# Kernel tuning notes

Hardware: AMD Instinct MI355X
Metric: run time of the kernel (lower is better)

## Reference

```python
import jax, jax.numpy as jnp
import numpy as np

T = 4.0          # kd_T
PATCH_NUM = 16
MASK_NUM = 4
P = PATCH_NUM - MASK_NUM  # 12
B = 4096
D_IN = 640
D = 128


def embed(x, w1, b1, w2, b2):
    # Linear -> ReLU -> Linear -> L2 normalize over features
    h = jax.nn.relu(x @ w1.T + b1)
    y = h @ w2.T + b2
    norm = jnp.sqrt(jnp.sum(y * y, axis=1, keepdims=True))
    return y / norm


def kl_rows(y_s, y_t):
    # Matches KLDiv: kl_div(log_softmax(y_s/T), softmax(y_t/T), 'batchmean') * T^2
    # over dim=0 of a 1-D vector -> sum / D. Vectorized over leading dims.
    ls = jax.nn.log_softmax(y_s / T, axis=-1)
    lt = jax.nn.log_softmax(y_t / T, axis=-1)
    pt = jnp.exp(lt)
    return jnp.sum(pt * (lt - ls), axis=-1) / y_s.shape[-1] * (T * T)


def setup_inputs() -> dict:
    key = jax.random.key(0)
    ks = jax.random.split(key, 11)
    return {
        "ebg": jax.random.normal(ks[0], (B, D_IN), jnp.float32),
        "ebp": jax.random.normal(ks[1], (P * B, D_IN), jnp.float32),
        "labelsg": jax.random.randint(ks[2], (B,), 0, 64),
        "glo_w1": jax.random.normal(ks[3], (D, D_IN), jnp.float32) * 0.04,
        "glo_b1": jax.random.normal(ks[4], (D,), jnp.float32) * 0.02,
        "glo_w2": jax.random.normal(ks[5], (D, D), jnp.float32) * 0.09,
        "glo_b2": jax.random.normal(ks[6], (D,), jnp.float32) * 0.02,
        "pat_w1": jax.random.normal(ks[7], (D, D_IN), jnp.float32) * 0.04,
        "pat_b1": jax.random.normal(ks[8], (D,), jnp.float32) * 0.02,
        "pat_w2": jax.random.normal(ks[9], (D, D), jnp.float32) * 0.09,
        "pat_b2": jax.random.normal(ks[10], (D,), jnp.float32) * 0.02,
    }


def reference(ebg, ebp, labelsg, glo_w1, glo_b1, glo_w2, glo_b2,
              pat_w1, pat_b1, pat_w2, pat_b2):
    sg = jax.lax.stop_gradient
    g = embed(ebg, glo_w1, glo_b1, glo_w2, glo_b2)          # [B, D]
    p = embed(ebp, pat_w1, pat_b1, pat_w2, pat_b2)          # [P*B, D]
    p = p.reshape(P, B, D)
    p_bar = p.mean(axis=0)                                  # [B, D]

    # soft_dil_loss: symmetric KL between g[b] and p_bar[b]
    dil = jnp.sum(kl_rows(g, sg(p_bar)) + kl_rows(p_bar, sg(g)))

    # soft_dcl_loss: symmetric KL between (g[b]-p[b,l])^2 and (p_bar[b]-p[b,l])^2
    p_bt = jnp.transpose(p, (1, 0, 2))                      # [B, P, D]
    d1 = (g[:, None, :] - p_bt) ** 2                        # [B, P, D]
    d2 = (p_bar[:, None, :] - p_bt) ** 2                    # [B, P, D]
    dcl = jnp.sum(kl_rows(d1, sg(d2)) + kl_rows(d2, sg(d1))) / P

    return (dil, dcl)
```

## Files before the change

### kernel.cpp

```cpp
#include <hip/hip_runtime.h>
#include <math.h>

#define B_    4096
#define DIN   640
#define DD    128
#define PP    12
#define INV_T 0.25f

typedef __bf16 bft;
typedef __attribute__((ext_vector_type(8))) __bf16 bf16x8;
typedef __attribute__((ext_vector_type(4))) float fx4;

__global__ __launch_bounds__(256) void prep_kernel(
    const float* __restrict__ gw1, const float* __restrict__ pw1,
    const float* __restrict__ gw2, const float* __restrict__ pw2,
    bft* __restrict__ w1hg, bft* __restrict__ w1lg,
    bft* __restrict__ w1hp, bft* __restrict__ w1lp,
    bft* __restrict__ w2hg, bft* __restrict__ w2lg,
    bft* __restrict__ w2hp, bft* __restrict__ w2lp)
{
  int idx = blockIdx.x * 256 + threadIdx.x;
  const float* src; bft *dh, *dl; int off;
  if (idx < 81920)       { src = gw1; dh = w1hg; dl = w1lg; off = idx; }
  else if (idx < 163840) { src = pw1; dh = w1hp; dl = w1lp; off = idx - 81920; }
  else if (idx < 180224) { src = gw2; dh = w2hg; dl = w2lg; off = idx - 163840; }
  else                   { src = pw2; dh = w2hp; dl = w2lp; off = idx - 180224; }
  float x = src[off];
  bft h = (bft)x;
  dh[off] = h;
  dl[off] = (bft)(x - (float)h);
}

__global__ __launch_bounds__(256, 2) void embed_kernel(
    const float* __restrict__ ebg, const float* __restrict__ ebp,
    const bft* __restrict__ w1hg, const bft* __restrict__ w1lg, const float* __restrict__ b1g,
    const bft* __restrict__ w2hg, const bft* __restrict__ w2lg, const float* __restrict__ b2g,
    const bft* __restrict__ w1hp, const bft* __restrict__ w1lp, const float* __restrict__ b1p,
    const bft* __restrict__ w2hp, const bft* __restrict__ w2lp, const float* __restrict__ b2p,
    float* __restrict__ outg, float* __restrict__ outp)
{
  __shared__ bft hsm[2 * 128 * 128];
  bft* hhi = hsm;
  bft* hlo = hsm + 128 * 128;
  float* halfsq = (float*)hsm;

  const int t = threadIdx.x;
  const int w = t >> 6, lane = t & 63;
  const int wm = w >> 1, wn = w & 1;
  const int ln = lane & 15, quad = lane >> 4;

  const float *X, *B1, *B2;
  const bft *W1H, *W1L, *W2H, *W2L;
  float* Y;
  long m0;
  if (blockIdx.x < 32) {
    X = ebg; W1H = w1hg; W1L = w1lg; B1 = b1g; W2H = w2hg; W2L = w2lg; B2 = b2g;
    Y = outg; m0 = (long)blockIdx.x * 128;
  } else {
    X = ebp; W1H = w1hp; W1L = w1lp; B1 = b1p; W2H = w2hp; W2L = w2lp; B2 = b2p;
    Y = outp; m0 = (long)(blockIdx.x - 32) * 128;
  }

  const float* px[4];
#pragma unroll
  for (int mt = 0; mt < 4; mt++)
    px[mt] = X + (size_t)(m0 + wm * 64 + mt * 16 + ln) * DIN + quad * 8;

  const bft *p1h[4], *p1l[4];
#pragma unroll
  for (int nt = 0; nt < 4; nt++) {
    int n = wn * 64 + nt * 16 + ln;
    p1h[nt] = W1H + (size_t)n * DIN + quad * 8;
    p1l[nt] = W1L + (size_t)n * DIN + quad * 8;
  }

  fx4 acc[4][4];
#pragma unroll
  for (int mt = 0; mt < 4; mt++)
#pragma unroll
    for (int nt = 0; nt < 4; nt++) acc[mt][nt] = (fx4){0.f, 0.f, 0.f, 0.f};

#define LOADX(xlo, xhi, koff)                              \
  _Pragma("unroll")                                        \
  for (int mt = 0; mt < 4; mt++) {                         \
    xlo[mt] = *(const fx4*)(px[mt] + (koff));              \
    xhi[mt] = *(const fx4*)(px[mt] + (koff) + 4);          \
  }

#define LOADW(wh, wl, koff)                                \
  _Pragma("unroll")                                        \
  for (int nt = 0; nt < 4; nt++) {                         \
    wh[nt] = *(const bf16x8*)(p1h[nt] + (koff));           \
    wl[nt] = *(const bf16x8*)(p1l[nt] + (koff));           \
  }

#define PH1CHUNK(xlo, xhi, wh, wl)                                                     \
  {                                                                                    \
    bf16x8 ah[4], al[4];                                                               \
    _Pragma("unroll")                                                                  \
    for (int mt = 0; mt < 4; mt++) {                                                   \
      _Pragma("unroll")                                                                \
      for (int j = 0; j < 4; j++) {                                                    \
        float xv = xlo[mt][j];                                                         \
        bft hh = (bft)xv;                                                              \
        ah[mt][j] = hh;                                                                \
        al[mt][j] = (bft)(xv - (float)hh);                                             \
        float yv = xhi[mt][j];                                                         \
        bft hh2 = (bft)yv;                                                             \
        ah[mt][4 + j] = hh2;                                                           \
        al[mt][4 + j] = (bft)(yv - (float)hh2);                                        \
      }                                                                                \
    }                                                                                  \
    _Pragma("unroll")                                                                  \
    for (int mt = 0; mt < 4; mt++)                                                     \
      _Pragma("unroll")                                                                \
      for (int nt = 0; nt < 4; nt++) {                                                 \
        acc[mt][nt] = __builtin_amdgcn_mfma_f32_16x16x32_bf16(ah[mt], wh[nt], acc[mt][nt], 0, 0, 0); \
        acc[mt][nt] = __builtin_amdgcn_mfma_f32_16x16x32_bf16(al[mt], wh[nt], acc[mt][nt], 0, 0, 0); \
        acc[mt][nt] = __builtin_amdgcn_mfma_f32_16x16x32_bf16(ah[mt], wl[nt], acc[mt][nt], 0, 0, 0); \
      }                                                                                \
  }

  fx4 xla[4], xha[4], xlb[4], xhb[4];
  bf16x8 wha[4], wla[4], whb[4], wlb[4];
  LOADX(xla, xha, 0)
  LOADW(wha, wla, 0)
#pragma unroll 1
  for (int kc = 0; kc < 20; kc += 2) {
    const int k1 = (kc + 1) * 32;
    LOADX(xlb, xhb, k1)
    LOADW(whb, wlb, k1)
    PH1CHUNK(xla, xha, wha, wla)
    if (kc < 18) {
      const int k2 = (kc + 2) * 32;
      LOADX(xla, xha, k2)
      LOADW(wha, wla, k2)
    }
    PH1CHUNK(xlb, xhb, whb, wlb)
  }

#pragma unroll
  for (int nt = 0; nt < 4; nt++) {
    float bv = B1[wn * 64 + nt * 16 + ln];
    int c8 = wn * 8 + nt * 2 + (ln >> 3);
    int c7 = ln & 7;
#pragma unroll
    for (int mt = 0; mt < 4; mt++) {
#pragma unroll
      for (int r = 0; r < 4; r++) {
        float v = fmaxf(acc[mt][nt][r] + bv, 0.f);
        bft h = (bft)v;
        bft l = (bft)(v - (float)h);
        int m = wm * 64 + mt * 16 + quad * 4 + r;
        int addr = m * 128 + ((c8 ^ (m & 15)) << 3) + c7;
        hhi[addr] = h;
        hlo[addr] = l;
      }
    }
  }

  const bft *p2h[4], *p2l[4];
#pragma unroll
  for (int nt = 0; nt < 4; nt++) {
    int n = wn * 64 + nt * 16 + ln;
    p2h[nt] = W2H + (size_t)n * DD + quad * 8;
    p2l[nt] = W2L + (size_t)n * DD + quad * 8;
  }
  fx4 acc2[4][4];
#pragma unroll
  for (int nt = 0; nt < 4; nt++) {
    float bv = B2[wn * 64 + nt * 16 + ln];
#pragma unroll
    for (int mt = 0; mt < 4; mt++) acc2[mt][nt] = (fx4){bv, bv, bv, bv};
  }

#define LOADW2(wh, wl, koff)                               \
  _Pragma("unroll")                                        \
  for (int nt = 0; nt < 4; nt++) {                         \
    wh[nt] = *(const bf16x8*)(p2h[nt] + (koff));           \
    wl[nt] = *(const bf16x8*)(p2l[nt] + (koff));           \
  }

#define PH2CHUNK(kcv, wh, wl)                                                          \
  {                                                                                    \
    bf16x8 ah2[4], al2[4];                                                             \
    _Pragma("unroll")                                                                  \
    for (int mt = 0; mt < 4; mt++) {                                                   \
      int m = wm * 64 + mt * 16 + ln;                                                  \
      int c8 = ((kcv) * 4 + quad) ^ (m & 15);                                          \
      ah2[mt] = *(const bf16x8*)&hhi[m * 128 + (c8 << 3)];                             \
      al2[mt] = *(const bf16x8*)&hlo[m * 128 + (c8 << 3)];                             \
    }                                                                                  \
    _Pragma("unroll")                                                                  \
    for (int mt = 0; mt < 4; mt++)                                                     \
      _Pragma("unroll")                                                                \
      for (int nt = 0; nt < 4; nt++) {                                                 \
        acc2[mt][nt] = __builtin_amdgcn_mfma_f32_16x16x32_bf16(ah2[mt], wh[nt], acc2[mt][nt], 0, 0, 0); \
        acc2[mt][nt] = __builtin_amdgcn_mfma_f32_16x16x32_bf16(al2[mt], wh[nt], acc2[mt][nt], 0, 0, 0); \
        acc2[mt][nt] = __builtin_amdgcn_mfma_f32_16x16x32_bf16(ah2[mt], wl[nt], acc2[mt][nt], 0, 0, 0); \
      }                                                                                \
  }

  bf16x8 q2ha[4], q2la[4], q2hb[4], q2lb[4];
  LOADW2(q2ha, q2la, 0)
  __syncthreads();
  LOADW2(q2hb, q2lb, 32)
  PH2CHUNK(0, q2ha, q2la)
  LOADW2(q2ha, q2la, 64)
  PH2CHUNK(1, q2hb, q2lb)
  LOADW2(q2hb, q2lb, 96)
  PH2CHUNK(2, q2ha, q2la)
  PH2CHUNK(3, q2hb, q2lb)
  __syncthreads();

#pragma unroll
  for (int mt = 0; mt < 4; mt++) {
#pragma unroll
    for (int r = 0; r < 4; r++) {
      float s = 0.f;
#pragma unroll
      for (int nt = 0; nt < 4; nt++) { float v = acc2[mt][nt][r]; s += v * v; }
      s += __shfl_xor(s, 1, 64);
      s += __shfl_xor(s, 2, 64);
      s += __shfl_xor(s, 4, 64);
      s += __shfl_xor(s, 8, 64);
      if (ln == 0) halfsq[(wm * 64 + mt * 16 + quad * 4 + r) * 2 + wn] = s;
    }
  }
  __syncthreads();
#pragma unroll
  for (int mt = 0; mt < 4; mt++) {
#pragma unroll
    for (int r = 0; r < 4; r++) {
      int row = wm * 64 + mt * 16 + quad * 4 + r;
      float rinv = 1.0f / sqrtf(halfsq[row * 2] + halfsq[row * 2 + 1]);
#pragma unroll
      for (int nt = 0; nt < 4; nt++)
        Y[(m0 + row) * DD + wn * 64 + nt * 16 + ln] = acc2[mt][nt][r] * rinv;
    }
  }
}

__device__ __forceinline__ float sym_kl_row(float au0, float au1, float av0, float av1)
{
  float eu0 = __expf(au0), eu1 = __expf(au1);
  float ev0 = __expf(av0), ev1 = __expf(av1);
  float su = eu0 + eu1, sv = ev0 + ev1;
#pragma unroll
  for (int o = 32; o > 0; o >>= 1) {
    su += __shfl_xor(su, o, 64);
    sv += __shfl_xor(sv, o, 64);
  }
  float ru = 1.0f / su, rv = 1.0f / sv;
  float d0 = au0 - av0, d1 = au1 - av1;
  float part = (eu0 * ru - ev0 * rv) * d0 + (eu1 * ru - ev1 * rv) * d1;
#pragma unroll
  for (int o = 32; o > 0; o >>= 1) part += __shfl_xor(part, o, 64);
  return part;
}

__global__ __launch_bounds__(256) void loss_kernel(
    const float* __restrict__ g, const float* __restrict__ p,
    float* __restrict__ pdil, float* __restrict__ pdcl)
{
  __shared__ float wd[4], wc[4];
  int w = threadIdx.x >> 6, lane = threadIdx.x & 63;
  int b = blockIdx.x * 4 + w;
  float2 pl[PP];
  float sx = 0.f, sy = 0.f;
#pragma unroll
  for (int l = 0; l < PP; l++) {
    pl[l] = *(const float2*)&p[((size_t)l * B_ + b) * DD + lane * 2];
    sx += pl[l].x; sy += pl[l].y;
  }
  sx *= (1.0f / PP); sy *= (1.0f / PP);
  float2 gv = *(const float2*)&g[(size_t)b * DD + lane * 2];

  float dil = sym_kl_row(gv.x * INV_T, gv.y * INV_T, sx * INV_T, sy * INV_T) * 0.125f;

  float dcl = 0.f;
#pragma unroll
  for (int l = 0; l < PP; l++) {
    float u0 = (gv.x - pl[l].x) * (gv.x - pl[l].x) * INV_T;
    float u1 = (gv.y - pl[l].y) * (gv.y - pl[l].y) * INV_T;
    float v0 = (sx - pl[l].x) * (sx - pl[l].x) * INV_T;
    float v1 = (sy - pl[l].y) * (sy - pl[l].y) * INV_T;
    dcl += sym_kl_row(u0, u1, v0, v1);
  }
  dcl *= (1.0f / 96.0f);

  if (lane == 0) { wd[w] = dil; wc[w] = dcl; }
  __syncthreads();
  if (threadIdx.x == 0) pdil[blockIdx.x] = wd[0] + wd[1] + wd[2] + wd[3];
  if (threadIdx.x == 1) pdcl[blockIdx.x] = wc[0] + wc[1] + wc[2] + wc[3];
}

__global__ __launch_bounds__(256) void final_kernel(const float* __restrict__ pdil,
                                                    const float* __restrict__ pdcl,
                                                    float* __restrict__ out)
{
  __shared__ float red[8];
  int t = threadIdx.x;
  float s0 = 0.f, s1 = 0.f;
  for (int i = t; i < 1024; i += 256) { s0 += pdil[i]; s1 += pdcl[i]; }
#pragma unroll
  for (int o = 32; o > 0; o >>= 1) {
    s0 += __shfl_xor(s0, o, 64);
    s1 += __shfl_xor(s1, o, 64);
  }
  int wid = t >> 6, lane = t & 63;
  if (lane == 0) { red[wid] = s0; red[4 + wid] = s1; }
  __syncthreads();
  if (t == 0) out[0] = red[0] + red[1] + red[2] + red[3];
  if (t == 1) out[1] = red[4] + red[5] + red[6] + red[7];
}

extern "C" void kernel_launch(void* const* d_in, const int* in_sizes, int n_in,
                              void* d_out, int out_size, void* d_ws, size_t ws_size,
                              hipStream_t stream)
{
  const float* ebg = (const float*)d_in[0];
  const float* ebp = (const float*)d_in[1];
  const float* gw1 = (const float*)d_in[3];
  const float* gb1 = (const float*)d_in[4];
  const float* gw2 = (const float*)d_in[5];
  const float* gb2 = (const float*)d_in[6];
  const float* pw1 = (const float*)d_in[7];
  const float* pb1 = (const float*)d_in[8];
  const float* pw2 = (const float*)d_in[9];
  const float* pb2 = (const float*)d_in[10];
  float* out = (float*)d_out;

  float* ws   = (float*)d_ws;
  float* g    = ws;
  float* p    = g + (size_t)B_ * DD;
  float* pdil = p + (size_t)PP * B_ * DD;
  float* pdcl = pdil + 1024;
  bft* wb     = (bft*)(pdcl + 1024);
  bft* w1hg = wb;                 bft* w1lg = w1hg + 81920;
  bft* w1hp = w1lg + 81920;       bft* w1lp = w1hp + 81920;
  bft* w2hg = w1lp + 81920;       bft* w2lg = w2hg + 16384;
  bft* w2hp = w2lg + 16384;       bft* w2lp = w2hp + 16384;

  prep_kernel<<<768, 256, 0, stream>>>(gw1, pw1, gw2, pw2,
                                       w1hg, w1lg, w1hp, w1lp,
                                       w2hg, w2lg, w2hp, w2lp);
  embed_kernel<<<416, 256, 0, stream>>>(ebg, ebp,
                                        w1hg, w1lg, gb1, w2hg, w2lg, gb2,
                                        w1hp, w1lp, pb1, w2hp, w2lp, pb2,
                                        g, p);
  loss_kernel<<<B_ / 4, 256, 0, stream>>>(g, p, pdil, pdcl);
  final_kernel<<<1, 256, 0, stream>>>(pdil, pdcl, out);
}
```

Before: 294.0 us.

## Pipeline embed GEMM with async LDS staging of 16-row tiles and fragment-packed weights

Restructures the embed kernel so each block processes eight 16-row sub-tiles in sequence. Input rows are double-buffered into swizzled LDS via global_load_lds, and each wave computes 32 hidden columns of layer 1 and all 128 outputs of layer 2, which lets the row norm be reduced within a wave without a cross-wave LDS pass. Weights are pre-packed into an MFMA-fragment layout with hi and lo parts interleaved so lane loads are contiguous. The patch embeddings are written in [B, P, D] order so the loss kernel reads contiguous rows. The cost is more barriers per block and smaller per-wave MFMA tiles, which lowers reuse of each loaded operand.

```diff
diff --git a/kernel.cpp b/kernel.cpp
--- a/kernel.cpp
+++ b/kernel.cpp
@@ -11,233 +11,233 @@
 typedef __attribute__((ext_vector_type(8))) __bf16 bf16x8;
 typedef __attribute__((ext_vector_type(4))) float fx4;
 
+__device__ __forceinline__ void gload16(const float* gp, float* lp) {
+  __builtin_amdgcn_global_load_lds(
+      (const __attribute__((address_space(1))) unsigned int*)gp,
+      (__attribute__((address_space(3))) unsigned int*)lp,
+      16, 0, 0);
+}
+
 __global__ __launch_bounds__(256) void prep_kernel(
     const float* __restrict__ gw1, const float* __restrict__ pw1,
     const float* __restrict__ gw2, const float* __restrict__ pw2,
-    bft* __restrict__ w1hg, bft* __restrict__ w1lg,
-    bft* __restrict__ w1hp, bft* __restrict__ w1lp,
-    bft* __restrict__ w2hg, bft* __restrict__ w2lg,
-    bft* __restrict__ w2hp, bft* __restrict__ w2lp)
-{
-  int idx = blockIdx.x * 256 + threadIdx.x;
-  const float* src; bft *dh, *dl; int off;
-  if (idx < 81920)       { src = gw1; dh = w1hg; dl = w1lg; off = idx; }
-  else if (idx < 163840) { src = pw1; dh = w1hp; dl = w1lp; off = idx - 81920; }
-  else if (idx < 180224) { src = gw2; dh = w2hg; dl = w2lg; off = idx - 163840; }
-  else                   { src = pw2; dh = w2hp; dl = w2lp; off = idx - 180224; }
-  float x = src[off];
-  bft h = (bft)x;
-  dh[off] = h;
-  dl[off] = (bft)(x - (float)h);
+    bft* __restrict__ w1fg, bft* __restrict__ w1fp,
+    bft* __restrict__ w2fg, bft* __restrict__ w2fp)
+{
+  int id = blockIdx.x * 256 + threadIdx.x;
+  const float* src;
+  bft* dst;
+  int nt, kc, hl, lane, kstride;
+  if (id < 40960) {
+    const bool isg = (id < 20480);
+    int f = isg ? id : (id - 20480);
+    src = isg ? gw1 : pw1;
+    dst = isg ? w1fg : w1fp;
+    lane = f & 63;
+    int q2 = f >> 6;
+    hl = q2 & 1;
+    int q3 = q2 >> 1;
+    kc = q3 % 20; nt = q3 / 20;
+    kstride = DIN;
+    dst += ((size_t)(nt * 20 + kc) * 2 + hl) * 512 + lane * 8;
+  } else {
+    const bool isg = (id < 45056);
+    int f = isg ? (id - 40960) : (id - 45056);
+    src = isg ? gw2 : pw2;
+    dst = isg ? w2fg : w2fp;
+    lane = f & 63;
+    int q2 = f >> 6;
+    hl = q2 & 1;
+    int q3 = q2 >> 1;
+    kc = q3 & 3; nt = q3 >> 2;
+    kstride = DD;
+    dst += ((size_t)(nt * 4 + kc) * 2 + hl) * 512 + lane * 8;
+  }
+  int ln = lane & 15, quad = lane >> 4;
+  const float* s = src + (size_t)(nt * 16 + ln) * kstride + kc * 32 + quad * 8;
+#pragma unroll
+  for (int e = 0; e < 8; e++) {
+    float x = s[e];
+    bft h = (bft)x;
+    dst[e] = hl ? (bft)(x - (float)h) : h;
+  }
 }
 
 __global__ __launch_bounds__(256, 2) void embed_kernel(
     const float* __restrict__ ebg, const float* __restrict__ ebp,
-    const bft* __restrict__ w1hg, const bft* __restrict__ w1lg, const float* __restrict__ b1g,
-    const bft* __restrict__ w2hg, const bft* __restrict__ w2lg, const float* __restrict__ b2g,
-    const bft* __restrict__ w1hp, const bft* __restrict__ w1lp, const float* __restrict__ b1p,
-    const bft* __restrict__ w2hp, const bft* __restrict__ w2lp, const float* __restrict__ b2p,
+    const bft* __restrict__ w1fg, const float* __restrict__ b1g,
+    const bft* __restrict__ w2fg, const float* __restrict__ b2g,
+    const bft* __restrict__ w1fp, const float* __restrict__ b1p,
+    const bft* __restrict__ w2fp, const float* __restrict__ b2p,
     float* __restrict__ outg, float* __restrict__ outp)
 {
-  __shared__ bft hsm[2 * 128 * 128];
-  bft* hhi = hsm;
-  bft* hlo = hsm + 128 * 128;
-  float* halfsq = (float*)hsm;
+  __shared__ __align__(16) float xsm[2 * 10240];
 
   const int t = threadIdx.x;
   const int w = t >> 6, lane = t & 63;
-  const int wm = w >> 1, wn = w & 1;
   const int ln = lane & 15, quad = lane >> 4;
 
   const float *X, *B1, *B2;
-  const bft *W1H, *W1L, *W2H, *W2L;
+  const bft *W1F, *W2F;
   float* Y;
   long m0;
-  if (blockIdx.x < 32) {
-    X = ebg; W1H = w1hg; W1L = w1lg; B1 = b1g; W2H = w2hg; W2L = w2lg; B2 = b2g;
+  const bool isg = (blockIdx.x < 32);
+  if (isg) {
+    X = ebg; W1F = w1fg; B1 = b1g; W2F = w2fg; B2 = b2g;
     Y = outg; m0 = (long)blockIdx.x * 128;
   } else {
-    X = ebp; W1H = w1hp; W1L = w1lp; B1 = b1p; W2H = w2hp; W2L = w2lp; B2 = b2p;
+    X = ebp; W1F = w1fp; B1 = b1p; W2F = w2fp; B2 = b2p;
     Y = outp; m0 = (long)(blockIdx.x - 32) * 128;
   }
 
-  const float* px[4];
-#pragma unroll
-  for (int mt = 0; mt < 4; mt++)
-    px[mt] = X + (size_t)(m0 + wm * 64 + mt * 16 + ln) * DIN + quad * 8;
-
-  const bft *p1h[4], *p1l[4];
-#pragma unroll
-  for (int nt = 0; nt < 4; nt++) {
-    int n = wn * 64 + nt * 16 + ln;
-    p1h[nt] = W1H + (size_t)n * DIN + quad * 8;
-    p1l[nt] = W1L + (size_t)n * DIN + quad * 8;
-  }
-
-  fx4 acc[4][4];
-#pragma unroll
-  for (int mt = 0; mt < 4; mt++)
-#pragma unroll
-    for (int nt = 0; nt < 4; nt++) acc[mt][nt] = (fx4){0.f, 0.f, 0.f, 0.f};
-
-#define LOADX(xlo, xhi, koff)                              \
-  _Pragma("unroll")                                        \
-  for (int mt = 0; mt < 4; mt++) {                         \
-    xlo[mt] = *(const fx4*)(px[mt] + (koff));              \
-    xhi[mt] = *(const fx4*)(px[mt] + (koff) + 4);          \
-  }
-
-#define LOADW(wh, wl, koff)                                \
-  _Pragma("unroll")                                        \
-  for (int nt = 0; nt < 4; nt++) {                         \
-    wh[nt] = *(const bf16x8*)(p1h[nt] + (koff));           \
-    wl[nt] = *(const bf16x8*)(p1l[nt] + (koff));           \
-  }
-
-#define PH1CHUNK(xlo, xhi, wh, wl)                                                     \
-  {                                                                                    \
-    bf16x8 ah[4], al[4];                                                               \
-    _Pragma("unroll")                                                                  \
-    for (int mt = 0; mt < 4; mt++) {                                                   \
-      _Pragma("unroll")                                                                \
-      for (int j = 0; j < 4; j++) {                                                    \
-        float xv = xlo[mt][j];                                                         \
-        bft hh = (bft)xv;                                                              \
-        ah[mt][j] = hh;                                                                \
-        al[mt][j] = (bft)(xv - (float)hh);                                             \
-        float yv = xhi[mt][j];                                                         \
-        bft hh2 = (bft)yv;                                                             \
-        ah[mt][4 + j] = hh2;                                                           \
-        al[mt][4 + j] = (bft)(yv - (float)hh2);                                        \
-      }                                                                                \
-    }                                                                                  \
-    _Pragma("unroll")                                                                  \
-    for (int mt = 0; mt < 4; mt++)                                                     \
-      _Pragma("unroll")                                                                \
-      for (int nt = 0; nt < 4; nt++) {                                                 \
-        acc[mt][nt] = __builtin_amdgcn_mfma_f32_16x16x32_bf16(ah[mt], wh[nt], acc[mt][nt], 0, 0, 0); \
-        acc[mt][nt] = __builtin_amdgcn_mfma_f32_16x16x32_bf16(al[mt], wh[nt], acc[mt][nt], 0, 0, 0); \
-        acc[mt][nt] = __builtin_amdgcn_mfma_f32_16x16x32_bf16(ah[mt], wl[nt], acc[mt][nt], 0, 0, 0); \
-      }                                                                                \
-  }
-
-  fx4 xla[4], xha[4], xlb[4], xhb[4];
-  bf16x8 wha[4], wla[4], whb[4], wlb[4];
-  LOADX(xla, xha, 0)
-  LOADW(wha, wla, 0)
+  int soff[10];
+#pragma unroll
+  for (int j = 0; j < 10; j++) {
+    int pch = w * 640 + j * 64 + lane;
+    int r = pch / 160, c = pch - r * 160;
+    soff[j] = r * 640 + ((c ^ (r & 7)) << 2);
+  }
+
+#define STAGE(ts, slot)                                                     \
+  {                                                                          \
+    const float* xb_ = X + (size_t)(m0 + (ts) * 16) * DIN;                   \
+    float* ds_ = xsm + (slot) * 10240;                                       \
+    _Pragma("unroll")                                                        \
+    for (int j = 0; j < 10; j++)                                             \
+      gload16(xb_ + soff[j], ds_ + (w * 640 + j * 64 + lane) * 4);           \
+  }
+
+  float b1v[2], b2v[8];
+#pragma unroll
+  for (int nt = 0; nt < 2; nt++) b1v[nt] = B1[w * 32 + nt * 16 + ln];
+#pragma unroll
+  for (int n8 = 0; n8 < 8; n8++) b2v[n8] = B2[n8 * 16 + ln];
+
+  STAGE(0, 0)
+  STAGE(1, 1)
+
+#define EMBSTEP(s_, VMTOK)                                                   \
+  {                                                                          \
+    const int cur_ = (s_) & 1;                                               \
+    float* xslot = xsm + cur_ * 10240;                                       \
+    bft* hhi = (bft*)xslot;                                                  \
+    bft* hlo = hhi + 16 * 128;                                               \
+    asm volatile("s_waitcnt vmcnt(" VMTOK ") lgkmcnt(0)" ::: "memory");      \
+    __builtin_amdgcn_s_barrier();                                            \
+    __builtin_amdgcn_sched_barrier(0);                                       \
+    fx4 acc0 = (fx4){0.f, 0.f, 0.f, 0.f};                                    \
+    fx4 acc1 = (fx4){0.f, 0.f, 0.f, 0.f};                                    \
+    const bft* w1b = W1F + (size_t)(2 * w) * 20480 + lane * 8;               \
+    const float* xr = xslot + ln * 640;                                      \
+    _Pragma("unroll")                                                        \
+    for (int kc = 0; kc < 20; kc++) {                                        \
+      fx4 x0 = *(const fx4*)(xr + (((kc * 8 + quad * 2)     ^ (ln & 7)) << 2)); \
+      fx4 x1 = *(const fx4*)(xr + (((kc * 8 + quad * 2 + 1) ^ (ln & 7)) << 2)); \
+      bf16x8 ah, al;                                                         \
+      _Pragma("unroll")                                                      \
+      for (int j = 0; j < 4; j++) {                                          \
+        float xv = x0[j];                                                    \
+        bft hh = (bft)xv;                                                    \
+        ah[j] = hh;                                                          \
+        al[j] = (bft)(xv - (float)hh);                                       \
+        float yv = x1[j];                                                    \
+        bft hh2 = (bft)yv;                                                   \
+        ah[4 + j] = hh2;                                                     \
+        al[4 + j] = (bft)(yv - (float)hh2);                                  \
+      }                                                                      \
+      bf16x8 wh0 = *(const bf16x8*)(w1b + (kc * 2) * 512);                   \
+      bf16x8 wl0 = *(const bf16x8*)(w1b + (kc * 2 + 1) * 512);               \
+      bf16x8 wh1 = *(const bf16x8*)(w1b + 20480 + (kc * 2) * 512);           \
+      bf16x8 wl1 = *(const bf16x8*)(w1b + 20480 + (kc * 2 + 1) * 512);       \
+      acc0 = __builtin_amdgcn_mfma_f32_16x16x32_bf16(ah, wh0, acc0, 0, 0, 0); \
+      acc0 = __builtin_amdgcn_mfma_f32_16x16x32_bf16(al, wh0, acc0, 0, 0, 0); \
+      acc0 = __builtin_amdgcn_mfma_f32_16x16x32_bf16(ah, wl0, acc0, 0, 0, 0); \
+      acc1 = __builtin_amdgcn_mfma_f32_16x16x32_bf16(ah, wh1, acc1, 0, 0, 0); \
+      acc1 = __builtin_amdgcn_mfma_f32_16x16x32_bf16(al, wh1, acc1, 0, 0, 0); \
+      acc1 = __builtin_amdgcn_mfma_f32_16x16x32_bf16(ah, wl1, acc1, 0, 0, 0); \
+    }                                                                        \
+    asm volatile("s_waitcnt lgkmcnt(0)" ::: "memory");                       \
+    __builtin_amdgcn_s_barrier();                                            \
+    __builtin_amdgcn_sched_barrier(0);                                       \
+    _Pragma("unroll")                                                        \
+    for (int nt = 0; nt < 2; nt++) {                                         \
+      int ch = w * 4 + nt * 2 + (ln >> 3);                                   \
+      int c7 = ln & 7;                                                       \
+      fx4 a_ = nt ? acc1 : acc0;                                             \
+      _Pragma("unroll")                                                      \
+      for (int r = 0; r < 4; r++) {                                          \
+        float v = fmaxf(a_[r] + b1v[nt], 0.f);                               \
+        bft h = (bft)v;                                                      \
+        bft l = (bft)(v - (float)h);                                         \
+        int row = quad * 4 + r;                                              \
+        int addr = row * 128 + (((ch ^ row) & 15) << 3) + c7;                \
+        hhi[addr] = h;                                                       \
+        hlo[addr] = l;                                                       \
+      }                                                                      \
+    }                                                                        \
+    asm volatile("s_waitcnt lgkmcnt(0)" ::: "memory");                       \
+    __builtin_amdgcn_s_barrier();                                            \
+    __builtin_amdgcn_sched_barrier(0);                                       \
+    bf16x8 ah2[4], al2[4];                                                   \
+    _Pragma("unroll")                                                        \
+    for (int kc2 = 0; kc2 < 4; kc2++) {                                      \
+      int ch2 = (kc2 * 4 + quad) ^ ln;                                       \
+      ah2[kc2] = *(const bf16x8*)&hhi[ln * 128 + (ch2 << 3)];                \
+      al2[kc2] = *(const bf16x8*)&hlo[ln * 128 + (ch2 << 3)];                \
+    }                                                                        \
+    asm volatile("s_waitcnt lgkmcnt(0)" ::: "memory");                       \
+    __builtin_amdgcn_s_barrier();                                            \
+    __builtin_amdgcn_sched_barrier(0);                                       \
+    {                                                                        \
+      int ts_ = ((s_) + 2 <= 7) ? (s_) + 2 : (s_);                           \
+      STAGE(ts_, cur_)                                                       \
+    }                                                                        \
+    fx4 o[8];                                                                \
+    _Pragma("unroll")                                                        \
+    for (int n8 = 0; n8 < 8; n8++)                                           \
+      o[n8] = (fx4){b2v[n8], b2v[n8], b2v[n8], b2v[n8]};                     \
+    _Pragma("unroll")                                                        \
+    for (int n8 = 0; n8 < 8; n8++) {                                         \
+      const bft* w2b = W2F + (size_t)n8 * 4096 + lane * 8;                   \
+      _Pragma("unroll")                                                      \
+      for (int kc2 = 0; kc2 < 4; kc2++) {                                    \
+        bf16x8 wh = *(const bf16x8*)(w2b + (kc2 * 2) * 512);                 \
+        bf16x8 wl = *(const bf16x8*)(w2b + (kc2 * 2 + 1) * 512);             \
+        o[n8] = __builtin_amdgcn_mfma_f32_16x16x32_bf16(ah2[kc2], wh, o[n8], 0, 0, 0); \
+        o[n8] = __builtin_amdgcn_mfma_f32_16x16x32_bf16(al2[kc2], wh, o[n8], 0, 0, 0); \
+        o[n8] = __builtin_amdgcn_mfma_f32_16x16x32_bf16(ah2[kc2], wl, o[n8], 0, 0, 0); \
+      }                                                                      \
+    }                                                                        \
+    _Pragma("unroll")                                                        \
+    for (int r = 0; r < 4; r++) {                                            \
+      float sq = 0.f;                                                        \
+      _Pragma("unroll")                                                      \
+      for (int n8 = 0; n8 < 8; n8++) { float v = o[n8][r]; sq += v * v; }    \
+      sq += __shfl_xor(sq, 1, 64);                                           \
+      sq += __shfl_xor(sq, 2, 64);                                           \
+      sq += __shfl_xor(sq, 4, 64);                                           \
+      sq += __shfl_xor(sq, 8, 64);                                           \
+      float rinv = 1.0f / sqrtf(sq);                                         \
+      long R = m0 + (s_) * 16 + quad * 4 + r;                                \
+      _Pragma("unroll")                                                      \
+      for (int nt = 0; nt < 2; nt++) {                                       \
+        int n8 = 2 * w + nt;                                                 \
+        float val = o[n8][r] * rinv;                                         \
+        if (isg) {                                                           \
+          Y[R * DD + n8 * 16 + ln] = val;                                    \
+        } else {                                                             \
+          long l_ = R >> 12, b_ = R & 4095;                                  \
+          Y[(b_ * PP + l_) * DD + n8 * 16 + ln] = val;                       \
+        }                                                                    \
+      }                                                                      \
+    }                                                                        \
+  }
+
+  EMBSTEP(0, "10")
+  EMBSTEP(1, "63")
 #pragma unroll 1
-  for (int kc = 0; kc < 20; kc += 2) {
-    const int k1 = (kc + 1) * 32;
-    LOADX(xlb, xhb, k1)
-    LOADW(whb, wlb, k1)
-    PH1CHUNK(xla, xha, wha, wla)
-    if (kc < 18) {
-      const int k2 = (kc + 2) * 32;
-      LOADX(xla, xha, k2)
-      LOADW(wha, wla, k2)
-    }
-    PH1CHUNK(xlb, xhb, whb, wlb)
-  }
-
-#pragma unroll
-  for (int nt = 0; nt < 4; nt++) {
-    float bv = B1[wn * 64 + nt * 16 + ln];
-    int c8 = wn * 8 + nt * 2 + (ln >> 3);
-    int c7 = ln & 7;
-#pragma unroll
-    for (int mt = 0; mt < 4; mt++) {
-#pragma unroll
-      for (int r = 0; r < 4; r++) {
-        float v = fmaxf(acc[mt][nt][r] + bv, 0.f);
-        bft h = (bft)v;
-        bft l = (bft)(v - (float)h);
-        int m = wm * 64 + mt * 16 + quad * 4 + r;
-        int addr = m * 128 + ((c8 ^ (m & 15)) << 3) + c7;
-        hhi[addr] = h;
-        hlo[addr] = l;
-      }
-    }
-  }
-
-  const bft *p2h[4], *p2l[4];
-#pragma unroll
-  for (int nt = 0; nt < 4; nt++) {
-    int n = wn * 64 + nt * 16 + ln;
-    p2h[nt] = W2H + (size_t)n * DD + quad * 8;
-    p2l[nt] = W2L + (size_t)n * DD + quad * 8;
-  }
-  fx4 acc2[4][4];
-#pragma unroll
-  for (int nt = 0; nt < 4; nt++) {
-    float bv = B2[wn * 64 + nt * 16 + ln];
-#pragma unroll
-    for (int mt = 0; mt < 4; mt++) acc2[mt][nt] = (fx4){bv, bv, bv, bv};
-  }
-
-#define LOADW2(wh, wl, koff)                               \
-  _Pragma("unroll")                                        \
-  for (int nt = 0; nt < 4; nt++) {                         \
-    wh[nt] = *(const bf16x8*)(p2h[nt] + (koff));           \
-    wl[nt] = *(const bf16x8*)(p2l[nt] + (koff));           \
-  }
-
-#define PH2CHUNK(kcv, wh, wl)                                                          \
-  {                                                                                    \
-    bf16x8 ah2[4], al2[4];                                                             \
-    _Pragma("unroll")                                                                  \
-    for (int mt = 0; mt < 4; mt++) {                                                   \
-      int m = wm * 64 + mt * 16 + ln;                                                  \
-      int c8 = ((kcv) * 4 + quad) ^ (m & 15);                                          \
-      ah2[mt] = *(const bf16x8*)&hhi[m * 128 + (c8 << 3)];                             \
-      al2[mt] = *(const bf16x8*)&hlo[m * 128 + (c8 << 3)];                             \
-    }                                                                                  \
-    _Pragma("unroll")                                                                  \
-    for (int mt = 0; mt < 4; mt++)                                                     \
-      _Pragma("unroll")                                                                \
-      for (int nt = 0; nt < 4; nt++) {                                                 \
-        acc2[mt][nt] = __builtin_amdgcn_mfma_f32_16x16x32_bf16(ah2[mt], wh[nt], acc2[mt][nt], 0, 0, 0); \
-        acc2[mt][nt] = __builtin_amdgcn_mfma_f32_16x16x32_bf16(al2[mt], wh[nt], acc2[mt][nt], 0, 0, 0); \
-        acc2[mt][nt] = __builtin_amdgcn_mfma_f32_16x16x32_bf16(ah2[mt], wl[nt], acc2[mt][nt], 0, 0, 0); \
-      }                                                                                \
-  }
-
-  bf16x8 q2ha[4], q2la[4], q2hb[4], q2lb[4];
-  LOADW2(q2ha, q2la, 0)
-  __syncthreads();
-  LOADW2(q2hb, q2lb, 32)
-  PH2CHUNK(0, q2ha, q2la)
-  LOADW2(q2ha, q2la, 64)
-  PH2CHUNK(1, q2hb, q2lb)
-  LOADW2(q2hb, q2lb, 96)
-  PH2CHUNK(2, q2ha, q2la)
-  PH2CHUNK(3, q2hb, q2lb)
-  __syncthreads();
-
-#pragma unroll
-  for (int mt = 0; mt < 4; mt++) {
-#pragma unroll
-    for (int r = 0; r < 4; r++) {
-      float s = 0.f;
-#pragma unroll
-      for (int nt = 0; nt < 4; nt++) { float v = acc2[mt][nt][r]; s += v * v; }
-      s += __shfl_xor(s, 1, 64);
-      s += __shfl_xor(s, 2, 64);
-      s += __shfl_xor(s, 4, 64);
-      s += __shfl_xor(s, 8, 64);
-      if (ln == 0) halfsq[(wm * 64 + mt * 16 + quad * 4 + r) * 2 + wn] = s;
-    }
-  }
-  __syncthreads();
-#pragma unroll
-  for (int mt = 0; mt < 4; mt++) {
-#pragma unroll
-    for (int r = 0; r < 4; r++) {
-      int row = wm * 64 + mt * 16 + quad * 4 + r;
-      float rinv = 1.0f / sqrtf(halfsq[row * 2] + halfsq[row * 2 + 1]);
-#pragma unroll
-      for (int nt = 0; nt < 4; nt++)
-        Y[(m0 + row) * DD + wn * 64 + nt * 16 + ln] = acc2[mt][nt][r] * rinv;
-    }
+  for (int s = 2; s < 8; s++) {
+    EMBSTEP(s, "63")
   }
 }
 
@@ -270,7 +270,7 @@
   float sx = 0.f, sy = 0.f;
 #pragma unroll
   for (int l = 0; l < PP; l++) {
-    pl[l] = *(const float2*)&p[((size_t)l * B_ + b) * DD + lane * 2];
+    pl[l] = *(const float2*)&p[((size_t)b * PP + l) * DD + lane * 2];
     sx += pl[l].x; sy += pl[l].y;
   }
   sx *= (1.0f / PP); sy *= (1.0f / PP);
@@ -336,18 +336,17 @@
   float* p    = g + (size_t)B_ * DD;
   float* pdil = p + (size_t)PP * B_ * DD;
   float* pdcl = pdil + 1024;
-  bft* wb     = (bft*)(pdcl + 1024);
-  bft* w1hg = wb;                 bft* w1lg = w1hg + 81920;
-  bft* w1hp = w1lg + 81920;       bft* w1lp = w1hp + 81920;
-  bft* w2hg = w1lp + 81920;       bft* w2lg = w2hg + 16384;
-  bft* w2hp = w2lg + 16384;       bft* w2lp = w2hp + 16384;
-
-  prep_kernel<<<768, 256, 0, stream>>>(gw1, pw1, gw2, pw2,
-                                       w1hg, w1lg, w1hp, w1lp,
-                                       w2hg, w2lg, w2hp, w2lp);
+  bft* wb   = (bft*)(pdcl + 1024);
+  bft* w1fg = wb;
+  bft* w1fp = w1fg + 163840;
+  bft* w2fg = w1fp + 163840;
+  bft* w2fp = w2fg + 32768;
+
+  prep_kernel<<<192, 256, 0, stream>>>(gw1, pw1, gw2, pw2,
+                                       w1fg, w1fp, w2fg, w2fp);
   embed_kernel<<<416, 256, 0, stream>>>(ebg, ebp,
-                                        w1hg, w1lg, gb1, w2hg, w2lg, gb2,
-                                        w1hp, w1lp, pb1, w2hp, w2lp, pb2,
+                                        w1fg, gb1, w2fg, gb2,
+                                        w1fp, pb1, w2fp, pb2,
                                         g, p);
   loss_kernel<<<B_ / 4, 256, 0, stream>>>(g, p, pdil, pdcl);
   final_kernel<<<1, 256, 0, stream>>>(pdil, pdcl, out);
```

Result: slower. 575.5 us (+95.7%).
